# Kernel optimization log

Hardware: AMD Instinct MI355X
Metric: run time of the kernel (lower is better)

## Reference

```python
import jax, jax.numpy as jnp
import numpy as np

H = W = 64      # input_resolution
WS = 8          # window_size
SS = 4          # shift_size
DIM = 96
HEADS = 4
HEAD_DIM = DIM // HEADS
SCALE = HEAD_DIM ** -0.5
N = WS * WS     # tokens per window
EPS = 1e-5


def _rel_pos_index():
    # static (N, N) int index into the (2*WS-1)^2 bias table
    coords = np.stack(np.meshgrid(np.arange(WS), np.arange(WS), indexing='ij'))  # (2, WS, WS)
    cf = coords.reshape(2, -1)                       # (2, N)
    rel = (cf[:, :, None] - cf[:, None, :]).transpose(1, 2, 0)  # (N, N, 2)
    rel[:, :, 0] += WS - 1
    rel[:, :, 1] += WS - 1
    rel[:, :, 0] *= 2 * WS - 1
    return rel.sum(-1)                               # (N, N)


def _attn_mask():
    # static (nW, N, N) 0/-100 mask for shifted windows
    img = np.zeros((H, W))
    cnt = 0
    sl = (slice(0, -WS), slice(-WS, -SS), slice(-SS, None))
    for hs in sl:
        for ws_ in sl:
            img[hs, ws_] = cnt
            cnt += 1
    mw = img.reshape(H // WS, WS, W // WS, WS).transpose(0, 2, 1, 3).reshape(-1, N)
    diff = mw[:, None, :] - mw[:, :, None]
    return np.where(diff != 0, -100.0, 0.0).astype(np.float32)


_RPI = jnp.asarray(_rel_pos_index())
_MASK = jnp.asarray(_attn_mask())  # (nW, N, N)


def _layernorm(x, g, b):
    mu = jnp.mean(x, axis=-1, keepdims=True)
    var = jnp.mean(jnp.square(x - mu), axis=-1, keepdims=True)
    return (x - mu) * jax.lax.rsqrt(var + EPS) * g + b


def setup_inputs() -> dict:
    key = jax.random.key(0)
    ks = jax.random.split(key, 8)
    s = 0.02
    return {
        'x': jax.random.normal(ks[0], (64, H * W, DIM), jnp.float32),
        'norm1_g': jnp.ones((DIM,), jnp.float32),
        'norm1_b': jnp.zeros((DIM,), jnp.float32),
        'qkv_w': jax.random.normal(ks[1], (3 * DIM, DIM), jnp.float32) * s,
        'qkv_b': jnp.zeros((3 * DIM,), jnp.float32),
        'rel_bias_table': jax.random.normal(ks[2], ((2 * WS - 1) ** 2, HEADS), jnp.float32) * s,
        'proj_w': jax.random.normal(ks[3], (DIM, DIM), jnp.float32) * s,
        'proj_b': jnp.zeros((DIM,), jnp.float32),
        'norm2_g': jnp.ones((DIM,), jnp.float32),
        'norm2_b': jnp.zeros((DIM,), jnp.float32),
        'fc1_w': jax.random.normal(ks[4], (4 * DIM, DIM), jnp.float32) * s,
        'fc1_b': jnp.zeros((4 * DIM,), jnp.float32),
        'fc2_w': jax.random.normal(ks[5], (DIM, 4 * DIM), jnp.float32) * s,
        'fc2_b': jnp.zeros((DIM,), jnp.float32),
    }


def reference(x, norm1_g, norm1_b, qkv_w, qkv_b, rel_bias_table, proj_w, proj_b,
              norm2_g, norm2_b, fc1_w, fc1_b, fc2_w, fc2_b):
    B, L, C = x.shape
    nW = (H // WS) * (W // WS)
    shortcut = x

    h = _layernorm(x, norm1_g, norm1_b).reshape(B, H, W, C)
    h = jnp.roll(h, (-SS, -SS), axis=(1, 2))
    # window partition -> (B*nW, N, C)
    h = h.reshape(B, H // WS, WS, W // WS, WS, C).transpose(0, 1, 3, 2, 4, 5)
    h = h.reshape(B * nW, N, C)

    qkv = h @ qkv_w.T + qkv_b                                   # (B_, N, 3C)
    qkv = qkv.reshape(B * nW, N, 3, HEADS, HEAD_DIM).transpose(2, 0, 3, 1, 4)
    q, k, v = qkv[0] * SCALE, qkv[1], qkv[2]                    # (B_, heads, N, hd)

    attn = jnp.einsum('whnd,whmd->whnm', q, k)                  # (B_, heads, N, N)
    bias = rel_bias_table[_RPI.reshape(-1)].reshape(N, N, HEADS).transpose(2, 0, 1)
    attn = attn + bias[None]
    attn = attn.reshape(B, nW, HEADS, N, N) + _MASK[None, :, None]
    attn = jax.nn.softmax(attn.reshape(B * nW, HEADS, N, N), axis=-1)

    out = jnp.einsum('whnm,whmd->whnd', attn, v)                # (B_, heads, N, hd)
    out = out.transpose(0, 2, 1, 3).reshape(B * nW, N, C)
    out = out @ proj_w.T + proj_b

    # window reverse + un-shift
    out = out.reshape(B, H // WS, W // WS, WS, WS, C).transpose(0, 1, 3, 2, 4, 5)
    out = out.reshape(B, H, W, C)
    out = jnp.roll(out, (SS, SS), axis=(1, 2)).reshape(B, L, C)

    x = shortcut + out
    h2 = _layernorm(x, norm2_g, norm2_b)
    h2 = jax.nn.gelu(h2 @ fc1_w.T + fc1_b, approximate=False)
    h2 = h2 @ fc2_w.T + fc2_b
    return x + h2
```

## Files before the change

### kernel.cpp

```cpp
#include <hip/hip_runtime.h>
#include <hip/hip_fp16.h>
#include <math.h>

typedef _Float16 half_t;
typedef _Float16 half8 __attribute__((ext_vector_type(8)));
typedef float f32x4 __attribute__((ext_vector_type(4)));

#define MFMA(a, b, c) __builtin_amdgcn_mfma_f32_16x16x32_f16((a), (b), (c), 0, 0, 0)

static constexpr float kScale = 0.2041241452319315f;
static constexpr int RS   = 104;
static constexpr int QSTR = 200;
static constexpr int VTS  = 72;
static constexpr int H1S  = 392;

__global__ __launch_bounds__(256) void k_convert(const float* __restrict__ qkv_w,
                                                 const float* __restrict__ proj_w,
                                                 const float* __restrict__ fc1_w,
                                                 const float* __restrict__ fc2_w,
                                                 const float* __restrict__ tbl,
                                                 half_t* __restrict__ wbuf,
                                                 float* __restrict__ biasT) {
  int i = blockIdx.x * 256 + threadIdx.x;
  if (i < 27648)        wbuf[i] = (half_t)qkv_w[i];
  else if (i < 36864)   wbuf[i] = (half_t)proj_w[i - 27648];
  else if (i < 73728)   wbuf[i] = (half_t)fc1_w[i - 36864];
  else if (i < 110592)  wbuf[i] = (half_t)fc2_w[i - 73728];
  else if (biasT != nullptr) {
    int j = i - 110592;
    int h = j >> 12, rem = j & 4095;
    int ii = rem >> 6, jj = rem & 63;
    int ih = ii >> 3, iw = ii & 7, jh = jj >> 3, jw = jj & 7;
    biasT[j] = tbl[((ih - jh + 7) * 15 + (iw - jw + 7)) * 4 + h];
  }
}

__global__ __launch_bounds__(256, 3) void k_swin(
    const float* __restrict__ x,
    const float* __restrict__ n1g, const float* __restrict__ n1b,
    const half_t* __restrict__ qkvw, const float* __restrict__ qkv_b,
    const float* __restrict__ tbl_g, const float* __restrict__ biasT,
    const half_t* __restrict__ projw, const float* __restrict__ proj_b,
    const float* __restrict__ n2g, const float* __restrict__ n2b,
    const half_t* __restrict__ fc1w, const float* __restrict__ fc1b,
    const half_t* __restrict__ fc2w, const float* __restrict__ fc2b,
    float* __restrict__ out) {
  __shared__ __attribute__((aligned(16))) unsigned char smem[52736];
  half_t* qbuf = (half_t*)smem;
  half_t* h1h  = (half_t*)smem;
  half_t* vT   = (half_t*)(smem + 25600);
  half_t* rbuf = (half_t*)(smem + 25600);
  half_t* hn   = (half_t*)(smem + 39424);
  half_t* xn   = (half_t*)(smem + 39424);

  int tid = threadIdx.x;
  int wave = tid >> 6, lane = tid & 63;
  int l15 = lane & 15, quad = lane >> 4;
  int blk = blockIdx.x;
  int bb = blk >> 6, wh = (blk >> 3) & 7, ww = blk & 7;

  {
    int tok = wave * 16 + l15;
    int sr = (wh * 8 + (tok >> 3) + 4) & 63;
    int sc = (ww * 8 + (tok & 7) + 4) & 63;
    const float* rp = x + ((size_t)bb * 4096 + sr * 64 + sc) * 96;
    float v[24];
    float s1 = 0.f, s2 = 0.f;
#pragma unroll
    for (int kt = 0; kt < 3; ++kt) {
      float4 a = *(const float4*)(rp + kt * 32 + quad * 8);
      float4 b = *(const float4*)(rp + kt * 32 + quad * 8 + 4);
      v[kt*8+0]=a.x; v[kt*8+1]=a.y; v[kt*8+2]=a.z; v[kt*8+3]=a.w;
      v[kt*8+4]=b.x; v[kt*8+5]=b.y; v[kt*8+6]=b.z; v[kt*8+7]=b.w;
    }
#pragma unroll
    for (int c = 0; c < 24; ++c) { s1 += v[c]; s2 += v[c] * v[c]; }
    s1 += __shfl_xor(s1, 16); s1 += __shfl_xor(s1, 32);
    s2 += __shfl_xor(s2, 16); s2 += __shfl_xor(s2, 32);
    float mu = s1 * (1.f / 96.f);
    float inv = rsqrtf(fmaxf(s2 * (1.f / 96.f) - mu * mu, 0.f) + 1e-5f);
#pragma unroll
    for (int kt = 0; kt < 3; ++kt) {
      int c0 = kt * 32 + quad * 8;
      float4 g0 = *(const float4*)(n1g + c0);
      float4 g1 = *(const float4*)(n1g + c0 + 4);
      float4 b0 = *(const float4*)(n1b + c0);
      float4 b1 = *(const float4*)(n1b + c0 + 4);
      float gg[8] = {g0.x,g0.y,g0.z,g0.w,g1.x,g1.y,g1.z,g1.w};
      float bv[8] = {b0.x,b0.y,b0.z,b0.w,b1.x,b1.y,b1.z,b1.w};
      half8 hh;
#pragma unroll
      for (int j = 0; j < 8; ++j)
        hh[j] = (half_t)((v[kt*8+j] - mu) * inv * gg[j] + bv[j]);
      *(half8*)(&hn[tok * RS + kt * 32 + quad * 8]) = hh;
    }
  }
  __syncthreads();

  {
    half8 af[4][3];
#pragma unroll
    for (int g = 0; g < 4; ++g)
#pragma unroll
      for (int kt = 0; kt < 3; ++kt)
        af[g][kt] = *(const half8*)(&hn[(g * 16 + l15) * RS + kt * 32 + quad * 8]);
    for (int t = wave; t < 18; t += 4) {
      int n0 = t * 16 + l15;
      const half_t* wp = qkvw + (size_t)n0 * 96 + quad * 8;
      half8 b0 = *(const half8*)(wp);
      half8 b1 = *(const half8*)(wp + 32);
      half8 b2 = *(const half8*)(wp + 64);
      f32x4 acc[4] = {{0,0,0,0},{0,0,0,0},{0,0,0,0},{0,0,0,0}};
#pragma unroll
      for (int g = 0; g < 4; ++g) acc[g] = MFMA(af[g][0], b0, acc[g]);
#pragma unroll
      for (int g = 0; g < 4; ++g) acc[g] = MFMA(af[g][1], b1, acc[g]);
#pragma unroll
      for (int g = 0; g < 4; ++g) acc[g] = MFMA(af[g][2], b2, acc[g]);
      float bias = qkv_b[n0];
      if (t < 12) {
        float sc_ = (t < 6) ? kScale : 1.f;
#pragma unroll
        for (int g = 0; g < 4; ++g)
#pragma unroll
          for (int r = 0; r < 4; ++r)
            qbuf[(g * 16 + quad * 4 + r) * QSTR + n0] = (half_t)((acc[g][r] + bias) * sc_);
      } else {
        int vc = n0 - 192;
        int hd = vc / 24, c = vc - hd * 24;
#pragma unroll
        for (int g = 0; g < 4; ++g)
#pragma unroll
          for (int r = 0; r < 4; ++r)
            vT[hd * 24 * VTS + c * VTS + g * 16 + quad * 4 + r] = (half_t)(acc[g][r] + bias);
      }
    }
  }
  __syncthreads();

  {
    int head = wave;
    const half8 z8 = {};
    half8 kb[4], vb[2][2];
#pragma unroll
    for (int nt = 0; nt < 4; ++nt) {
      half8 t = *(const half8*)(&qbuf[(nt * 16 + l15) * QSTR + 96 + head * 24 + quad * 8]);
      kb[nt] = (quad < 3) ? t : z8;
    }
#pragma unroll
    for (int nt = 0; nt < 2; ++nt)
#pragma unroll
      for (int kt = 0; kt < 2; ++kt)
        vb[nt][kt] = *(const half8*)(&vT[head * 24 * VTS + (nt * 16 + l15) * VTS + kt * 32 + quad * 8]);

    int rj[4], jh_[4], jw_[4];
#pragma unroll
    for (int nt = 0; nt < 4; ++nt) {
      int j = nt * 16 + l15;
      jh_[nt] = j >> 3; jw_[nt] = j & 7;
      int rr = wh * 8 + jh_[nt], cc = ww * 8 + jw_[nt];
      rj[nt] = ((rr < 56) ? 0 : ((rr < 60) ? 1 : 2)) * 3 + ((cc < 56) ? 0 : ((cc < 60) ? 1 : 2));
    }

    half_t* pb = vT + head * 24 * VTS;
    f32x4 oacc[4][2];

#pragma unroll
    for (int g2 = 0; g2 < 4; ++g2) {
      half8 qt = *(const half8*)(&qbuf[(g2 * 16 + l15) * QSTR + head * 24 + quad * 8]);
      half8 qa = (quad < 3) ? qt : z8;
      f32x4 sv[4];
#pragma unroll
      for (int nt = 0; nt < 4; ++nt) {
        f32x4 a = {0, 0, 0, 0};
        sv[nt] = MFMA(qa, kb[nt], a);
      }
      float pinv[4];
#pragma unroll
      for (int r = 0; r < 4; ++r) {
        int i = g2 * 16 + quad * 4 + r;
        int ih = i >> 3, iw = i & 7;
        int rr = wh * 8 + ih, cc = ww * 8 + iw;
        int ri = ((rr < 56) ? 0 : ((rr < 60) ? 1 : 2)) * 3 + ((cc < 56) ? 0 : ((cc < 60) ? 1 : 2));
        float bvv[4];
        if (biasT != nullptr) {
          const float* bp = biasT + (head << 12) + (i << 6) + l15;
#pragma unroll
          for (int nt = 0; nt < 4; ++nt) bvv[nt] = bp[nt * 16];
        } else {
#pragma unroll
          for (int nt = 0; nt < 4; ++nt)
            bvv[nt] = tbl_g[((ih - jh_[nt] + 7) * 15 + (iw - jw_[nt] + 7)) * 4 + head];
        }
#pragma unroll
        for (int nt = 0; nt < 4; ++nt) {
          float val = sv[nt][r] + bvv[nt];
          if (ri != rj[nt]) val -= 100.f;
          sv[nt][r] = val;
        }
        float mx = fmaxf(fmaxf(sv[0][r], sv[1][r]), fmaxf(sv[2][r], sv[3][r]));
        mx = fmaxf(mx, __shfl_xor(mx, 1));
        mx = fmaxf(mx, __shfl_xor(mx, 2));
        mx = fmaxf(mx, __shfl_xor(mx, 4));
        mx = fmaxf(mx, __shfl_xor(mx, 8));
        float sum = 0.f;
#pragma unroll
        for (int nt = 0; nt < 4; ++nt) {
          float e = __expf(sv[nt][r] - mx);
          sv[nt][r] = e;
          sum += e;
        }
        sum += __shfl_xor(sum, 1);
        sum += __shfl_xor(sum, 2);
        sum += __shfl_xor(sum, 4);
        sum += __shfl_xor(sum, 8);
        pinv[r] = __builtin_amdgcn_rcpf(sum);
      }
#pragma unroll
      for (int nt = 0; nt < 4; ++nt)
#pragma unroll
        for (int r = 0; r < 4; ++r)
          pb[(quad * 4 + r) * VTS + nt * 16 + l15] = (half_t)(sv[nt][r] * pinv[r]);
      __builtin_amdgcn_sched_barrier(0);
      half8 pa0 = *(const half8*)(&pb[l15 * VTS + quad * 8]);
      half8 pa1 = *(const half8*)(&pb[l15 * VTS + 32 + quad * 8]);
#pragma unroll
      for (int nt = 0; nt < 2; ++nt) {
        f32x4 a = {0, 0, 0, 0};
        a = MFMA(pa0, vb[nt][0], a);
        a = MFMA(pa1, vb[nt][1], a);
        oacc[g2][nt] = a;
      }
    }
#pragma unroll
    for (int g2 = 0; g2 < 4; ++g2)
#pragma unroll
      for (int nt = 0; nt < 2; ++nt) {
        int c = nt * 16 + l15;
        if (c < 24)
#pragma unroll
          for (int r = 0; r < 4; ++r)
            qbuf[(g2 * 16 + quad * 4 + r) * QSTR + head * 24 + c] = (half_t)oacc[g2][nt][r];
      }
  }
  __syncthreads();

  {
    half8 oa[3];
#pragma unroll
    for (int kt = 0; kt < 3; ++kt)
      oa[kt] = *(const half8*)(&qbuf[(wave * 16 + l15) * QSTR + kt * 32 + quad * 8]);
    f32x4 acc[6];
#pragma unroll
    for (int t = 0; t < 6; ++t) {
      int n0 = t * 16 + l15;
      const half_t* wp = projw + (size_t)n0 * 96 + quad * 8;
      half8 b0 = *(const half8*)(wp);
      half8 b1 = *(const half8*)(wp + 32);
      half8 b2 = *(const half8*)(wp + 64);
      f32x4 a = {0, 0, 0, 0};
      a = MFMA(oa[0], b0, a);
      a = MFMA(oa[1], b1, a);
      a = MFMA(oa[2], b2, a);
      acc[t] = a;
    }
    float xv[6][4];
#pragma unroll
    for (int r = 0; r < 4; ++r) {
      int tok = wave * 16 + quad * 4 + r;
      int sr = (wh * 8 + (tok >> 3) + 4) & 63;
      int sc = (ww * 8 + (tok & 7) + 4) & 63;
      const float* xp = x + ((size_t)bb * 4096 + sr * 64 + sc) * 96 + l15;
#pragma unroll
      for (int t = 0; t < 6; ++t) xv[t][r] = xp[t * 16];
    }
    float rv[6][4];
    float s1[4] = {0, 0, 0, 0}, s2[4] = {0, 0, 0, 0};
#pragma unroll
    for (int t = 0; t < 6; ++t) {
      float pbv = proj_b[t * 16 + l15];
#pragma unroll
      for (int r = 0; r < 4; ++r) {
        float vvv = xv[t][r] + acc[t][r] + pbv;
        rv[t][r] = vvv;
        s1[r] += vvv; s2[r] += vvv * vvv;
      }
    }
    float mu[4], nv[4];
#pragma unroll
    for (int r = 0; r < 4; ++r) {
      s1[r] += __shfl_xor(s1[r], 1); s1[r] += __shfl_xor(s1[r], 2);
      s1[r] += __shfl_xor(s1[r], 4); s1[r] += __shfl_xor(s1[r], 8);
      s2[r] += __shfl_xor(s2[r], 1); s2[r] += __shfl_xor(s2[r], 2);
      s2[r] += __shfl_xor(s2[r], 4); s2[r] += __shfl_xor(s2[r], 8);
      mu[r] = s1[r] * (1.f / 96.f);
      nv[r] = rsqrtf(fmaxf(s2[r] * (1.f / 96.f) - mu[r] * mu[r], 0.f) + 1e-5f);
    }
#pragma unroll
    for (int t = 0; t < 6; ++t) {
      int n0 = t * 16 + l15;
      float gv = n2g[n0], bv = n2b[n0];
#pragma unroll
      for (int r = 0; r < 4; ++r) {
        int row = wave * 16 + quad * 4 + r;
        rbuf[row * RS + n0] = (half_t)rv[t][r];
        xn[row * RS + n0] = (half_t)((rv[t][r] - mu[r]) * nv[r] * gv + bv);
      }
    }
  }
  __syncthreads();

  for (int hb = 0; hb < 2; ++hb) {
    {
      half8 a5[2][3];
#pragma unroll
      for (int g2 = 0; g2 < 2; ++g2)
#pragma unroll
        for (int kt = 0; kt < 3; ++kt)
          a5[g2][kt] = *(const half8*)(&xn[((hb * 2 + g2) * 16 + l15) * RS + kt * 32 + quad * 8]);
      for (int t = wave; t < 24; t += 4) {
        int n0 = t * 16 + l15;
        const half_t* wp = fc1w + (size_t)n0 * 96 + quad * 8;
        half8 b0 = *(const half8*)(wp);
        half8 b1 = *(const half8*)(wp + 32);
        half8 b2 = *(const half8*)(wp + 64);
        f32x4 acc[2] = {{0,0,0,0},{0,0,0,0}};
#pragma unroll
        for (int g2 = 0; g2 < 2; ++g2) acc[g2] = MFMA(a5[g2][0], b0, acc[g2]);
#pragma unroll
        for (int g2 = 0; g2 < 2; ++g2) acc[g2] = MFMA(a5[g2][1], b1, acc[g2]);
#pragma unroll
        for (int g2 = 0; g2 < 2; ++g2) acc[g2] = MFMA(a5[g2][2], b2, acc[g2]);
        float bias = fc1b[n0];
#pragma unroll
        for (int g2 = 0; g2 < 2; ++g2)
#pragma unroll
          for (int r = 0; r < 4; ++r) {
            float vvv = acc[g2][r] + bias;
            float u = vvv * (1.5957691216f + 0.1427096322f * vvv * vvv);
            float g = vvv * __builtin_amdgcn_rcpf(1.f + __expf(-u));
            h1h[(g2 * 16 + quad * 4 + r) * H1S + n0] = (half_t)g;
          }
      }
    }
    __syncthreads();
    {
      int rt = wave >> 1, chh = wave & 1;
      half8 a2[12];
#pragma unroll
      for (int kt = 0; kt < 12; ++kt)
        a2[kt] = *(const half8*)(&h1h[(rt * 16 + l15) * H1S + kt * 32 + quad * 8]);
#pragma unroll
      for (int i = 0; i < 3; ++i) {
        int t = chh * 3 + i;
        f32x4 acc = {0, 0, 0, 0};
#pragma unroll
        for (int kt = 0; kt < 12; ++kt) {
          half8 bf = *(const half8*)(fc2w + (size_t)(t * 16 + l15) * 384 + kt * 32 + quad * 8);
          acc = MFMA(a2[kt], bf, acc);
        }
        int col = t * 16 + l15;
        float bias = fc2b[col];
#pragma unroll
        for (int r = 0; r < 4; ++r) {
          int tok = hb * 32 + rt * 16 + quad * 4 + r;
          int sr = (wh * 8 + (tok >> 3) + 4) & 63;
          int sc = (ww * 8 + (tok & 7) + 4) & 63;
          size_t fidx = ((size_t)bb * 4096 + sr * 64 + sc) * 96 + col;
          out[fidx] = (float)rbuf[tok * RS + col] + acc[r] + bias;
        }
      }
    }
    __syncthreads();
  }
}

extern "C" void kernel_launch(void* const* d_in, const int* in_sizes, int n_in,
                              void* d_out, int out_size, void* d_ws, size_t ws_size,
                              hipStream_t stream) {
  const float* x      = (const float*)d_in[0];
  const float* n1g    = (const float*)d_in[1];
  const float* n1b    = (const float*)d_in[2];
  const float* qkv_w  = (const float*)d_in[3];
  const float* qkv_b  = (const float*)d_in[4];
  const float* rtbl   = (const float*)d_in[5];
  const float* proj_w = (const float*)d_in[6];
  const float* proj_b = (const float*)d_in[7];
  const float* n2g    = (const float*)d_in[8];
  const float* n2b    = (const float*)d_in[9];
  const float* fc1_w  = (const float*)d_in[10];
  const float* fc1_b  = (const float*)d_in[11];
  const float* fc2_w  = (const float*)d_in[12];
  const float* fc2_b  = (const float*)d_in[13];
  float* out = (float*)d_out;

  if (ws_size < 221184) return;
  half_t* wbuf = (half_t*)d_ws;
  float* biasT = (ws_size >= 221184 + 65536) ? (float*)((char*)d_ws + 221184) : nullptr;

  k_convert<<<496, 256, 0, stream>>>(qkv_w, proj_w, fc1_w, fc2_w, rtbl, wbuf, biasT);
  k_swin<<<4096, 256, 0, stream>>>(x, n1g, n1b, wbuf, qkv_b, rtbl, biasT,
                                   wbuf + 27648, proj_b, n2g, n2b,
                                   wbuf + 36864, fc1_b, wbuf + 73728, fc2_b, out);
}
```

Measured before the change: 436.5 us.

## Software-pipeline weight loads across phases and use lightweight LDS barriers

Global weight fragments for the QKV, proj, fc1 and fc2 GEMMs are now prefetched into registers one or two tiles ahead, and loads are issued before the preceding barrier so their latency overlaps LDS work and MFMA. The residual x reload, norm2 parameters and the relative-position bias values are also hoisted before barriers. __syncthreads is replaced by an inline s_waitcnt lgkmcnt(0) plus s_barrier, which does not wait on outstanding global loads. The cost is much higher register pressure (W3 structs, 12-entry fc2 buffers, a 64-float bias array), which risks spills or lower occupancy.

```diff
diff --git a/kernel.cpp b/kernel.cpp
--- a/kernel.cpp
+++ b/kernel.cpp
@@ -7,12 +7,147 @@
 typedef float f32x4 __attribute__((ext_vector_type(4)));
 
 #define MFMA(a, b, c) __builtin_amdgcn_mfma_f32_16x16x32_f16((a), (b), (c), 0, 0, 0)
+#define BARRIER() asm volatile("s_waitcnt lgkmcnt(0)\n\ts_barrier" ::: "memory")
 
 static constexpr float kScale = 0.2041241452319315f;
 static constexpr int RS   = 104;
 static constexpr int QSTR = 200;
 static constexpr int VTS  = 72;
 static constexpr int H1S  = 392;
+
+struct W3 { half8 b0, b1, b2; float bias; };
+
+__device__ __forceinline__ W3 ld_w3(const half_t* w, const float* bv, int n0, int qo) {
+  W3 r;
+  const half_t* wp = w + (size_t)n0 * 96 + qo;
+  r.b0 = *(const half8*)(wp);
+  r.b1 = *(const half8*)(wp + 32);
+  r.b2 = *(const half8*)(wp + 64);
+  r.bias = bv[n0];
+  return r;
+}
+
+__device__ __forceinline__ void qkv_tile(const W3& w, int t, int l15, int quad,
+                                         const half8 (&af)[4][3],
+                                         half_t* qbuf, half_t* vT) {
+  f32x4 acc[4] = {{0,0,0,0},{0,0,0,0},{0,0,0,0},{0,0,0,0}};
+#pragma unroll
+  for (int g = 0; g < 4; ++g) acc[g] = MFMA(af[g][0], w.b0, acc[g]);
+#pragma unroll
+  for (int g = 0; g < 4; ++g) acc[g] = MFMA(af[g][1], w.b1, acc[g]);
+#pragma unroll
+  for (int g = 0; g < 4; ++g) acc[g] = MFMA(af[g][2], w.b2, acc[g]);
+  int n0 = t * 16 + l15;
+  if (t < 12) {
+    float sc_ = (t < 6) ? kScale : 1.f;
+#pragma unroll
+    for (int g = 0; g < 4; ++g)
+#pragma unroll
+      for (int r = 0; r < 4; ++r)
+        qbuf[(g * 16 + quad * 4 + r) * QSTR + n0] = (half_t)((acc[g][r] + w.bias) * sc_);
+  } else {
+    int vc = n0 - 192;
+    int hd = vc / 24, c = vc - hd * 24;
+#pragma unroll
+    for (int g = 0; g < 4; ++g)
+#pragma unroll
+      for (int r = 0; r < 4; ++r)
+        vT[hd * 24 * VTS + c * VTS + g * 16 + quad * 4 + r] = (half_t)(acc[g][r] + w.bias);
+  }
+}
+
+__device__ __forceinline__ void fc1_tile(const W3& w, int t, int l15, int quad,
+                                         const half8 (&a5)[2][3], half_t* h1h) {
+  f32x4 a0 = {0,0,0,0}, a1 = {0,0,0,0};
+  a0 = MFMA(a5[0][0], w.b0, a0); a1 = MFMA(a5[1][0], w.b0, a1);
+  a0 = MFMA(a5[0][1], w.b1, a0); a1 = MFMA(a5[1][1], w.b1, a1);
+  a0 = MFMA(a5[0][2], w.b2, a0); a1 = MFMA(a5[1][2], w.b2, a1);
+  int n0 = t * 16 + l15;
+#pragma unroll
+  for (int g2 = 0; g2 < 2; ++g2) {
+    const f32x4& ac = g2 ? a1 : a0;
+#pragma unroll
+    for (int r = 0; r < 4; ++r) {
+      float vvv = ac[r] + w.bias;
+      float u = vvv * (1.5957691216f + 0.1427096322f * vvv * vvv);
+      float g = vvv * __builtin_amdgcn_rcpf(1.f + __expf(-u));
+      h1h[(g2 * 16 + quad * 4 + r) * H1S + n0] = (half_t)g;
+    }
+  }
+}
+
+__device__ __forceinline__ void fc2_ld(const half_t* fc2w, int t, int l15, int qo,
+                                       half8 (&bf)[12]) {
+#pragma unroll
+  for (int kt = 0; kt < 12; ++kt)
+    bf[kt] = *(const half8*)(fc2w + (size_t)(t * 16 + l15) * 384 + kt * 32 + qo);
+}
+
+__device__ __forceinline__ void fc2_tile(const half8 (&a2)[12], const half8 (&bf)[12],
+                                         int t, int hb, int rt, int l15, int quad,
+                                         int wh, int ww, int bb,
+                                         const float* fc2b, const half_t* rbuf,
+                                         float* out) {
+  f32x4 acc = {0,0,0,0};
+#pragma unroll
+  for (int kt = 0; kt < 12; ++kt) acc = MFMA(a2[kt], bf[kt], acc);
+  int col = t * 16 + l15;
+  float bias = fc2b[col];
+#pragma unroll
+  for (int r = 0; r < 4; ++r) {
+    int tok = hb * 32 + rt * 16 + quad * 4 + r;
+    int sr = (wh * 8 + (tok >> 3) + 4) & 63;
+    int sc = (ww * 8 + (tok & 7) + 4) & 63;
+    out[((size_t)bb * 4096 + sr * 64 + sc) * 96 + col] = (float)rbuf[tok * RS + col] + acc[r] + bias;
+  }
+}
+
+__device__ __forceinline__ void p5_pass(int hb, int wave, int l15, int quad, int qo, int chh,
+                                        const half_t* xn, half_t* h1h,
+                                        const half_t* fc1w, const float* fc1b,
+                                        const half_t* fc2w,
+                                        W3& f1A, W3& f1B, half8 (&bfA)[12]) {
+  half8 a5[2][3];
+#pragma unroll
+  for (int g2 = 0; g2 < 2; ++g2)
+#pragma unroll
+    for (int kt = 0; kt < 3; ++kt)
+      a5[g2][kt] = *(const half8*)(&xn[((hb * 2 + g2) * 16 + l15) * RS + kt * 32 + quad * 8]);
+  W3 f1C = ld_w3(fc1w, fc1b, (wave + 8) * 16 + l15, qo);
+  fc1_tile(f1A, wave, l15, quad, a5, h1h);
+  f1A = ld_w3(fc1w, fc1b, (wave + 12) * 16 + l15, qo);
+  fc1_tile(f1B, wave + 4, l15, quad, a5, h1h);
+  f1B = ld_w3(fc1w, fc1b, (wave + 16) * 16 + l15, qo);
+  fc1_tile(f1C, wave + 8, l15, quad, a5, h1h);
+  f1C = ld_w3(fc1w, fc1b, (wave + 20) * 16 + l15, qo);
+  fc1_tile(f1A, wave + 12, l15, quad, a5, h1h);
+  fc2_ld(fc2w, chh * 3 + 0, l15, qo, bfA);
+  fc1_tile(f1B, wave + 16, l15, quad, a5, h1h);
+  fc1_tile(f1C, wave + 20, l15, quad, a5, h1h);
+}
+
+__device__ __forceinline__ void p6_pass(int hb, int wave, int l15, int quad, int qo, int chh,
+                                        int wh, int ww, int bb, bool pre_fc1,
+                                        const half_t* h1h, const half_t* rbuf,
+                                        const half_t* fc2w, const float* fc2b,
+                                        const half_t* fc1w, const float* fc1b,
+                                        float* out,
+                                        W3& f1A, W3& f1B, half8 (&bfA)[12], half8 (&bfB)[12]) {
+  int rt = wave >> 1;
+  half8 a2[12];
+#pragma unroll
+  for (int kt = 0; kt < 12; ++kt)
+    a2[kt] = *(const half8*)(&h1h[(rt * 16 + l15) * H1S + kt * 32 + quad * 8]);
+  fc2_ld(fc2w, chh * 3 + 1, l15, qo, bfB);
+  fc2_tile(a2, bfA, chh * 3 + 0, hb, rt, l15, quad, wh, ww, bb, fc2b, rbuf, out);
+  fc2_ld(fc2w, chh * 3 + 2, l15, qo, bfA);
+  fc2_tile(a2, bfB, chh * 3 + 1, hb, rt, l15, quad, wh, ww, bb, fc2b, rbuf, out);
+  if (pre_fc1) {
+    f1A = ld_w3(fc1w, fc1b, wave * 16 + l15, qo);
+    f1B = ld_w3(fc1w, fc1b, (wave + 4) * 16 + l15, qo);
+  }
+  fc2_tile(a2, bfA, chh * 3 + 2, hb, rt, l15, quad, wh, ww, bb, fc2b, rbuf, out);
+}
 
 __global__ __launch_bounds__(256) void k_convert(const float* __restrict__ qkv_w,
                                                  const float* __restrict__ proj_w,
@@ -56,23 +191,29 @@
   int tid = threadIdx.x;
   int wave = tid >> 6, lane = tid & 63;
   int l15 = lane & 15, quad = lane >> 4;
+  int qo = quad * 8, chh = wave & 1;
   int blk = blockIdx.x;
   int bb = blk >> 6, wh = (blk >> 3) & 7, ww = blk & 7;
 
+  float v[24];
   {
     int tok = wave * 16 + l15;
     int sr = (wh * 8 + (tok >> 3) + 4) & 63;
     int sc = (ww * 8 + (tok & 7) + 4) & 63;
     const float* rp = x + ((size_t)bb * 4096 + sr * 64 + sc) * 96;
-    float v[24];
-    float s1 = 0.f, s2 = 0.f;
 #pragma unroll
     for (int kt = 0; kt < 3; ++kt) {
-      float4 a = *(const float4*)(rp + kt * 32 + quad * 8);
-      float4 b = *(const float4*)(rp + kt * 32 + quad * 8 + 4);
+      float4 a = *(const float4*)(rp + kt * 32 + qo);
+      float4 b = *(const float4*)(rp + kt * 32 + qo + 4);
       v[kt*8+0]=a.x; v[kt*8+1]=a.y; v[kt*8+2]=a.z; v[kt*8+3]=a.w;
       v[kt*8+4]=b.x; v[kt*8+5]=b.y; v[kt*8+6]=b.z; v[kt*8+7]=b.w;
     }
+  }
+  W3 qA = ld_w3(qkvw, qkv_b, wave * 16 + l15, qo);
+  W3 qB = ld_w3(qkvw, qkv_b, (wave + 4) * 16 + l15, qo);
+  {
+    int tok = wave * 16 + l15;
+    float s1 = 0.f, s2 = 0.f;
 #pragma unroll
     for (int c = 0; c < 24; ++c) { s1 += v[c]; s2 += v[c] * v[c]; }
     s1 += __shfl_xor(s1, 16); s1 += __shfl_xor(s1, 32);
@@ -81,7 +222,7 @@
     float inv = rsqrtf(fmaxf(s2 * (1.f / 96.f) - mu * mu, 0.f) + 1e-5f);
 #pragma unroll
     for (int kt = 0; kt < 3; ++kt) {
-      int c0 = kt * 32 + quad * 8;
+      int c0 = kt * 32 + qo;
       float4 g0 = *(const float4*)(n1g + c0);
       float4 g1 = *(const float4*)(n1g + c0 + 4);
       float4 b0 = *(const float4*)(n1b + c0);
@@ -92,66 +233,54 @@
 #pragma unroll
       for (int j = 0; j < 8; ++j)
         hh[j] = (half_t)((v[kt*8+j] - mu) * inv * gg[j] + bv[j]);
-      *(half8*)(&hn[tok * RS + kt * 32 + quad * 8]) = hh;
-    }
-  }
-  __syncthreads();
+      *(half8*)(&hn[tok * RS + kt * 32 + qo]) = hh;
+    }
+  }
+  BARRIER();
 
   {
+    W3 qC = ld_w3(qkvw, qkv_b, (wave + 8) * 16 + l15, qo);
     half8 af[4][3];
 #pragma unroll
     for (int g = 0; g < 4; ++g)
 #pragma unroll
       for (int kt = 0; kt < 3; ++kt)
-        af[g][kt] = *(const half8*)(&hn[(g * 16 + l15) * RS + kt * 32 + quad * 8]);
-    for (int t = wave; t < 18; t += 4) {
-      int n0 = t * 16 + l15;
-      const half_t* wp = qkvw + (size_t)n0 * 96 + quad * 8;
-      half8 b0 = *(const half8*)(wp);
-      half8 b1 = *(const half8*)(wp + 32);
-      half8 b2 = *(const half8*)(wp + 64);
-      f32x4 acc[4] = {{0,0,0,0},{0,0,0,0},{0,0,0,0},{0,0,0,0}};
-#pragma unroll
-      for (int g = 0; g < 4; ++g) acc[g] = MFMA(af[g][0], b0, acc[g]);
-#pragma unroll
-      for (int g = 0; g < 4; ++g) acc[g] = MFMA(af[g][1], b1, acc[g]);
-#pragma unroll
-      for (int g = 0; g < 4; ++g) acc[g] = MFMA(af[g][2], b2, acc[g]);
-      float bias = qkv_b[n0];
-      if (t < 12) {
-        float sc_ = (t < 6) ? kScale : 1.f;
-#pragma unroll
-        for (int g = 0; g < 4; ++g)
-#pragma unroll
-          for (int r = 0; r < 4; ++r)
-            qbuf[(g * 16 + quad * 4 + r) * QSTR + n0] = (half_t)((acc[g][r] + bias) * sc_);
-      } else {
-        int vc = n0 - 192;
-        int hd = vc / 24, c = vc - hd * 24;
-#pragma unroll
-        for (int g = 0; g < 4; ++g)
-#pragma unroll
-          for (int r = 0; r < 4; ++r)
-            vT[hd * 24 * VTS + c * VTS + g * 16 + quad * 4 + r] = (half_t)(acc[g][r] + bias);
-      }
-    }
-  }
-  __syncthreads();
+        af[g][kt] = *(const half8*)(&hn[(g * 16 + l15) * RS + kt * 32 + qo]);
+    qkv_tile(qA, wave, l15, quad, af, qbuf, vT);
+    qA = ld_w3(qkvw, qkv_b, (wave + 12) * 16 + l15, qo);
+    qkv_tile(qB, wave + 4, l15, quad, af, qbuf, vT);
+    if (wave < 2) qB = ld_w3(qkvw, qkv_b, (wave + 16) * 16 + l15, qo);
+    qkv_tile(qC, wave + 8, l15, quad, af, qbuf, vT);
+    qkv_tile(qA, wave + 12, l15, quad, af, qbuf, vT);
+    if (wave < 2) qkv_tile(qB, wave + 16, l15, quad, af, qbuf, vT);
+  }
+  int head = wave;
+  float bt[4][16];
+  if (biasT != nullptr) {
+#pragma unroll
+    for (int g2 = 0; g2 < 4; ++g2)
+#pragma unroll
+      for (int r = 0; r < 4; ++r) {
+        const float* bp = biasT + (head << 12) + ((g2 * 16 + quad * 4 + r) << 6) + l15;
+#pragma unroll
+        for (int nt = 0; nt < 4; ++nt) bt[g2][r * 4 + nt] = bp[nt * 16];
+      }
+  }
+  BARRIER();
 
   {
-    int head = wave;
     const half8 z8 = {};
     half8 kb[4], vb[2][2];
 #pragma unroll
     for (int nt = 0; nt < 4; ++nt) {
-      half8 t = *(const half8*)(&qbuf[(nt * 16 + l15) * QSTR + 96 + head * 24 + quad * 8]);
+      half8 t = *(const half8*)(&qbuf[(nt * 16 + l15) * QSTR + 96 + head * 24 + qo]);
       kb[nt] = (quad < 3) ? t : z8;
     }
 #pragma unroll
     for (int nt = 0; nt < 2; ++nt)
 #pragma unroll
       for (int kt = 0; kt < 2; ++kt)
-        vb[nt][kt] = *(const half8*)(&vT[head * 24 * VTS + (nt * 16 + l15) * VTS + kt * 32 + quad * 8]);
+        vb[nt][kt] = *(const half8*)(&vT[head * 24 * VTS + (nt * 16 + l15) * VTS + kt * 32 + qo]);
 
     int rj[4], jh_[4], jw_[4];
 #pragma unroll
@@ -167,7 +296,7 @@
 
 #pragma unroll
     for (int g2 = 0; g2 < 4; ++g2) {
-      half8 qt = *(const half8*)(&qbuf[(g2 * 16 + l15) * QSTR + head * 24 + quad * 8]);
+      half8 qt = *(const half8*)(&qbuf[(g2 * 16 + l15) * QSTR + head * 24 + qo]);
       half8 qa = (quad < 3) ? qt : z8;
       f32x4 sv[4];
 #pragma unroll
@@ -182,19 +311,12 @@
         int ih = i >> 3, iw = i & 7;
         int rr = wh * 8 + ih, cc = ww * 8 + iw;
         int ri = ((rr < 56) ? 0 : ((rr < 60) ? 1 : 2)) * 3 + ((cc < 56) ? 0 : ((cc < 60) ? 1 : 2));
-        float bvv[4];
-        if (biasT != nullptr) {
-          const float* bp = biasT + (head << 12) + (i << 6) + l15;
-#pragma unroll
-          for (int nt = 0; nt < 4; ++nt) bvv[nt] = bp[nt * 16];
-        } else {
-#pragma unroll
-          for (int nt = 0; nt < 4; ++nt)
-            bvv[nt] = tbl_g[((ih - jh_[nt] + 7) * 15 + (iw - jw_[nt] + 7)) * 4 + head];
-        }
 #pragma unroll
         for (int nt = 0; nt < 4; ++nt) {
-          float val = sv[nt][r] + bvv[nt];
+          float bvv;
+          if (biasT != nullptr) bvv = bt[g2][r * 4 + nt];
+          else bvv = tbl_g[((ih - jh_[nt] + 7) * 15 + (iw - jw_[nt] + 7)) * 4 + head];
+          float val = sv[nt][r] + bvv;
           if (ri != rj[nt]) val -= 100.f;
           sv[nt][r] = val;
         }
@@ -222,8 +344,8 @@
         for (int r = 0; r < 4; ++r)
           pb[(quad * 4 + r) * VTS + nt * 16 + l15] = (half_t)(sv[nt][r] * pinv[r]);
       __builtin_amdgcn_sched_barrier(0);
-      half8 pa0 = *(const half8*)(&pb[l15 * VTS + quad * 8]);
-      half8 pa1 = *(const half8*)(&pb[l15 * VTS + 32 + quad * 8]);
+      half8 pa0 = *(const half8*)(&pb[l15 * VTS + qo]);
+      half8 pa1 = *(const half8*)(&pb[l15 * VTS + 32 + qo]);
 #pragma unroll
       for (int nt = 0; nt < 2; ++nt) {
         f32x4 a = {0, 0, 0, 0};
@@ -243,49 +365,48 @@
             qbuf[(g2 * 16 + quad * 4 + r) * QSTR + head * 24 + c] = (half_t)oacc[g2][nt][r];
       }
   }
-  __syncthreads();
+  W3 pw[6];
+#pragma unroll
+  for (int t = 0; t < 6; ++t) pw[t] = ld_w3(projw, proj_b, t * 16 + l15, qo);
+  float xv[6][4];
+#pragma unroll
+  for (int r = 0; r < 4; ++r) {
+    int tok2 = wave * 16 + quad * 4 + r;
+    int sr = (wh * 8 + (tok2 >> 3) + 4) & 63;
+    int sc = (ww * 8 + (tok2 & 7) + 4) & 63;
+    const float* xp = x + ((size_t)bb * 4096 + sr * 64 + sc) * 96 + l15;
+#pragma unroll
+    for (int t = 0; t < 6; ++t) xv[t][r] = xp[t * 16];
+  }
+  float gn2[6], bn2[6];
+#pragma unroll
+  for (int t = 0; t < 6; ++t) { gn2[t] = n2g[t * 16 + l15]; bn2[t] = n2b[t * 16 + l15]; }
+  BARRIER();
 
   {
     half8 oa[3];
 #pragma unroll
     for (int kt = 0; kt < 3; ++kt)
-      oa[kt] = *(const half8*)(&qbuf[(wave * 16 + l15) * QSTR + kt * 32 + quad * 8]);
+      oa[kt] = *(const half8*)(&qbuf[(wave * 16 + l15) * QSTR + kt * 32 + qo]);
     f32x4 acc[6];
 #pragma unroll
     for (int t = 0; t < 6; ++t) {
-      int n0 = t * 16 + l15;
-      const half_t* wp = projw + (size_t)n0 * 96 + quad * 8;
-      half8 b0 = *(const half8*)(wp);
-      half8 b1 = *(const half8*)(wp + 32);
-      half8 b2 = *(const half8*)(wp + 64);
       f32x4 a = {0, 0, 0, 0};
-      a = MFMA(oa[0], b0, a);
-      a = MFMA(oa[1], b1, a);
-      a = MFMA(oa[2], b2, a);
+      a = MFMA(oa[0], pw[t].b0, a);
+      a = MFMA(oa[1], pw[t].b1, a);
+      a = MFMA(oa[2], pw[t].b2, a);
       acc[t] = a;
-    }
-    float xv[6][4];
-#pragma unroll
-    for (int r = 0; r < 4; ++r) {
-      int tok = wave * 16 + quad * 4 + r;
-      int sr = (wh * 8 + (tok >> 3) + 4) & 63;
-      int sc = (ww * 8 + (tok & 7) + 4) & 63;
-      const float* xp = x + ((size_t)bb * 4096 + sr * 64 + sc) * 96 + l15;
-#pragma unroll
-      for (int t = 0; t < 6; ++t) xv[t][r] = xp[t * 16];
     }
     float rv[6][4];
     float s1[4] = {0, 0, 0, 0}, s2[4] = {0, 0, 0, 0};
 #pragma unroll
-    for (int t = 0; t < 6; ++t) {
-      float pbv = proj_b[t * 16 + l15];
+    for (int t = 0; t < 6; ++t)
 #pragma unroll
       for (int r = 0; r < 4; ++r) {
-        float vvv = xv[t][r] + acc[t][r] + pbv;
+        float vvv = xv[t][r] + acc[t][r] + pw[t].bias;
         rv[t][r] = vvv;
         s1[r] += vvv; s2[r] += vvv * vvv;
       }
-    }
     float mu[4], nv[4];
 #pragma unroll
     for (int r = 0; r < 4; ++r) {
@@ -299,80 +420,28 @@
 #pragma unroll
     for (int t = 0; t < 6; ++t) {
       int n0 = t * 16 + l15;
-      float gv = n2g[n0], bv = n2b[n0];
 #pragma unroll
       for (int r = 0; r < 4; ++r) {
         int row = wave * 16 + quad * 4 + r;
         rbuf[row * RS + n0] = (half_t)rv[t][r];
-        xn[row * RS + n0] = (half_t)((rv[t][r] - mu[r]) * nv[r] * gv + bv);
-      }
-    }
-  }
-  __syncthreads();
-
-  for (int hb = 0; hb < 2; ++hb) {
-    {
-      half8 a5[2][3];
-#pragma unroll
-      for (int g2 = 0; g2 < 2; ++g2)
-#pragma unroll
-        for (int kt = 0; kt < 3; ++kt)
-          a5[g2][kt] = *(const half8*)(&xn[((hb * 2 + g2) * 16 + l15) * RS + kt * 32 + quad * 8]);
-      for (int t = wave; t < 24; t += 4) {
-        int n0 = t * 16 + l15;
-        const half_t* wp = fc1w + (size_t)n0 * 96 + quad * 8;
-        half8 b0 = *(const half8*)(wp);
-        half8 b1 = *(const half8*)(wp + 32);
-        half8 b2 = *(const half8*)(wp + 64);
-        f32x4 acc[2] = {{0,0,0,0},{0,0,0,0}};
-#pragma unroll
-        for (int g2 = 0; g2 < 2; ++g2) acc[g2] = MFMA(a5[g2][0], b0, acc[g2]);
-#pragma unroll
-        for (int g2 = 0; g2 < 2; ++g2) acc[g2] = MFMA(a5[g2][1], b1, acc[g2]);
-#pragma unroll
-        for (int g2 = 0; g2 < 2; ++g2) acc[g2] = MFMA(a5[g2][2], b2, acc[g2]);
-        float bias = fc1b[n0];
-#pragma unroll
-        for (int g2 = 0; g2 < 2; ++g2)
-#pragma unroll
-          for (int r = 0; r < 4; ++r) {
-            float vvv = acc[g2][r] + bias;
-            float u = vvv * (1.5957691216f + 0.1427096322f * vvv * vvv);
-            float g = vvv * __builtin_amdgcn_rcpf(1.f + __expf(-u));
-            h1h[(g2 * 16 + quad * 4 + r) * H1S + n0] = (half_t)g;
-          }
-      }
-    }
-    __syncthreads();
-    {
-      int rt = wave >> 1, chh = wave & 1;
-      half8 a2[12];
-#pragma unroll
-      for (int kt = 0; kt < 12; ++kt)
-        a2[kt] = *(const half8*)(&h1h[(rt * 16 + l15) * H1S + kt * 32 + quad * 8]);
-#pragma unroll
-      for (int i = 0; i < 3; ++i) {
-        int t = chh * 3 + i;
-        f32x4 acc = {0, 0, 0, 0};
-#pragma unroll
-        for (int kt = 0; kt < 12; ++kt) {
-          half8 bf = *(const half8*)(fc2w + (size_t)(t * 16 + l15) * 384 + kt * 32 + quad * 8);
-          acc = MFMA(a2[kt], bf, acc);
-        }
-        int col = t * 16 + l15;
-        float bias = fc2b[col];
-#pragma unroll
-        for (int r = 0; r < 4; ++r) {
-          int tok = hb * 32 + rt * 16 + quad * 4 + r;
-          int sr = (wh * 8 + (tok >> 3) + 4) & 63;
-          int sc = (ww * 8 + (tok & 7) + 4) & 63;
-          size_t fidx = ((size_t)bb * 4096 + sr * 64 + sc) * 96 + col;
-          out[fidx] = (float)rbuf[tok * RS + col] + acc[r] + bias;
-        }
-      }
-    }
-    __syncthreads();
-  }
+        xn[row * RS + n0] = (half_t)((rv[t][r] - mu[r]) * nv[r] * gn2[t] + bn2[t]);
+      }
+    }
+  }
+  W3 f1A = ld_w3(fc1w, fc1b, wave * 16 + l15, qo);
+  W3 f1B = ld_w3(fc1w, fc1b, (wave + 4) * 16 + l15, qo);
+  half8 bfA[12], bfB[12];
+  BARRIER();
+
+  p5_pass(0, wave, l15, quad, qo, chh, xn, h1h, fc1w, fc1b, fc2w, f1A, f1B, bfA);
+  BARRIER();
+  p6_pass(0, wave, l15, quad, qo, chh, wh, ww, bb, true,
+          h1h, rbuf, fc2w, fc2b, fc1w, fc1b, out, f1A, f1B, bfA, bfB);
+  BARRIER();
+  p5_pass(1, wave, l15, quad, qo, chh, xn, h1h, fc1w, fc1b, fc2w, f1A, f1B, bfA);
+  BARRIER();
+  p6_pass(1, wave, l15, quad, qo, chh, wh, ww, bb, false,
+          h1h, rbuf, fc2w, fc2b, fc1w, fc1b, out, f1A, f1B, bfA, bfB);
 }
 
 extern "C" void kernel_launch(void* const* d_in, const int* in_sizes, int n_in,
```

Result: faster. 406.8 us (-6.8%).
